# Performance work log

Measured on AMD Instinct MI355X. Metric: run time of the kernel, lower is better.

Reference implementation:

```python
import jax, jax.numpy as jnp
import numpy as np
from functools import partial

B, N, C = 16, 10647, 80   # batch, total anchors (YOLOv3@416), num classes
K = 2048                  # max candidates kept per image before NMS
SCORE_THR = 0.5
IOU_THR = 0.5


def setup_inputs() -> dict:
    key = jax.random.key(0)
    # [B, N, 4+1+C]: xywh (normalized), objectness, class probs
    y_pred = jax.random.uniform(key, (B, N, 5 + C), dtype=jnp.float32)
    return {"y_pred": y_pred}


def _xywh_to_corners(b):
    x, y, w, h = b[..., 0], b[..., 1], b[..., 2], b[..., 3]
    return jnp.stack([x - w / 2, y - h / 2, x + w / 2, y + h / 2], axis=-1)


def _pairwise_iou(boxes):  # boxes [K,4] corners -> [K,K]
    x1, y1, x2, y2 = boxes[:, 0], boxes[:, 1], boxes[:, 2], boxes[:, 3]
    area = jnp.maximum(x2 - x1, 0.0) * jnp.maximum(y2 - y1, 0.0)
    ix1 = jnp.maximum(x1[:, None], x1[None, :])
    iy1 = jnp.maximum(y1[:, None], y1[None, :])
    ix2 = jnp.minimum(x2[:, None], x2[None, :])
    iy2 = jnp.minimum(y2[:, None], y2[None, :])
    inter = jnp.maximum(ix2 - ix1, 0.0) * jnp.maximum(iy2 - iy1, 0.0)
    union = area[:, None] + area[None, :] - inter
    return inter / jnp.maximum(union, 1e-9)


def _greedy_nms_keep(boxes, valid):  # boxes [K,4] sorted by score desc, valid [K] bool
    iou = _pairwise_iou(boxes)
    idxs = jnp.arange(K)

    def body(i, keep):
        suppress = keep[i] & (idxs > i) & (iou[i] > IOU_THR)
        return keep & ~suppress

    return jax.lax.fori_loop(0, K, body, valid)


def reference(y_pred):
    boxes_xywh = y_pred[..., :4]           # [B,N,4]
    obj = y_pred[..., 4]                   # [B,N]
    cls_probs = y_pred[..., 5:]            # [B,N,C]
    scores = obj * jnp.max(cls_probs, axis=-1)  # [B,N]

    # top-K candidates per image (sorted by score desc)
    scores_k, idx = jax.lax.top_k(scores, K)             # [B,K]
    boxes_k = jnp.take_along_axis(boxes_xywh, idx[:, :, None], axis=1)  # [B,K,4]
    corners = _xywh_to_corners(boxes_k)                  # [B,K,4]

    valid = scores_k > SCORE_THR                          # [B,K]
    # NMS keep mask is a non-differentiable selection
    keep = jax.vmap(_greedy_nms_keep)(
        jax.lax.stop_gradient(corners), valid)            # [B,K] bool
    keep_f = keep.astype(scores_k.dtype)

    out_boxes = corners * keep_f[:, :, None]
    out_scores = scores_k * keep_f
    return jnp.concatenate([out_boxes, out_scores[:, :, None]], axis=-1)  # [B,K,5]
```

## Files before the change

kernel.cpp:

```cpp
#include <hip/hip_runtime.h>

#define BATCH 16
#define NROW  10647
#define ROWF  85
#define NCLS  80
#define KTOP  2048
#define MPAD  16384
#define SCORE_THR 0.5f
#define IOU_THR   0.5f

typedef unsigned long long u64;
typedef unsigned int u32;

__device__ __forceinline__ u32 enc_f32(float f) {
    u32 u = __float_as_uint(f);
    return (u & 0x80000000u) ? ~u : (u | 0x80000000u);
}
__device__ __forceinline__ float dec_f32(u32 e) {
    u32 u = (e & 0x80000000u) ? (e & 0x7FFFFFFFu) : ~e;
    return __uint_as_float(u);
}
__device__ __forceinline__ float bcast(float v, int ii) {
    return __uint_as_float(__builtin_amdgcn_readlane(__float_as_uint(v), ii));
}
__device__ __forceinline__ u64 rl64(u64 v, int l) {
    u32 lo = __builtin_amdgcn_readlane((u32)(v & 0xFFFFFFFFull), l);
    u32 hi = __builtin_amdgcn_readlane((u32)(v >> 32), l);
    return ((u64)hi << 32) | (u64)lo;
}
__device__ __forceinline__ void gload_lds16(const void* g, void* lds) {
    __builtin_amdgcn_global_load_lds(
        (const __attribute__((address_space(1))) void*)g,
        (__attribute__((address_space(3))) void*)lds, 16, 0, 0);
}
__device__ __forceinline__ void bar_lds() {
    asm volatile("s_waitcnt lgkmcnt(0)" ::: "memory");
    __builtin_amdgcn_s_barrier();
    __builtin_amdgcn_sched_barrier(0);
}

template<int J>
__device__ __forceinline__ void reg_pass(u64 v[8], int tid, int k) {
    #pragma unroll
    for (int r = 0; r < 8; ++r) {
        if (!(r & J)) {
            bool desc = (((tid * 8 + r) & k) == 0);
            u64 a = v[r], b = v[r | J];
            u64 mx = a > b ? a : b, mn = a > b ? b : a;
            v[r]     = desc ? mx : mn;
            v[r | J] = desc ? mn : mx;
        }
    }
}

__device__ __forceinline__ void shfl_pass(u64 v[8], int tid, int k, int d) {
    const bool upper = (tid & d) == 0;
    const bool desc = (((tid * 8) & k) == 0);
    const bool keepmax = (desc == upper);
    #pragma unroll
    for (int r = 0; r < 8; ++r) {
        u64 pv = __shfl_xor(v[r], d);
        u64 mx = v[r] > pv ? v[r] : pv, mn = v[r] > pv ? pv : v[r];
        v[r] = keepmax ? mx : mn;
    }
}

__device__ __forceinline__ void lds_pass(u64 v[8], int tid, u64* sm, int k, int d) {
    __syncthreads();
    #pragma unroll
    for (int r = 0; r < 8; ++r) sm[r * 256 + tid] = v[r];
    __syncthreads();
    const bool upper = (tid & d) == 0;
    const bool desc = (((tid * 8) & k) == 0);
    const bool keepmax = (desc == upper);
    const int pt = tid ^ d;
    #pragma unroll
    for (int r = 0; r < 8; ++r) {
        u64 pv = sm[r * 256 + pt];
        u64 mx = v[r] > pv ? v[r] : pv, mn = v[r] > pv ? pv : v[r];
        v[r] = keepmax ? mx : mn;
    }
}

__device__ __forceinline__ void sort2048_desc(u64 v[8], int tid, u64* sm) {
    reg_pass<1>(v, tid, 2);
    reg_pass<2>(v, tid, 4); reg_pass<1>(v, tid, 4);
    for (int k = 8; k <= 2048; k <<= 1) {
        for (int j = k >> 1; j >= 8; j >>= 1) {
            int d = j >> 3;
            if (d <= 32) shfl_pass(v, tid, k, d);
            else         lds_pass(v, tid, sm, k, d);
        }
        reg_pass<4>(v, tid, k); reg_pass<2>(v, tid, k); reg_pass<1>(v, tid, k);
    }
}

__device__ __forceinline__ void cleanup2048_desc(u64 v[8], int tid, u64* sm) {
    lds_pass(v, tid, sm, 4096, 128);
    lds_pass(v, tid, sm, 4096, 64);
    for (int d = 32; d >= 1; d >>= 1) shfl_pass(v, tid, 4096, d);
    reg_pass<4>(v, tid, 4096); reg_pass<2>(v, tid, 4096); reg_pass<1>(v, tid, 4096);
}

__global__ void score_kernel(const float* __restrict__ yp, u64* __restrict__ keys) {
    __shared__ float tile[128 * ROWF];
    const int tileIdx = blockIdx.x;
    const int b = blockIdx.y;
    const int tid = threadIdx.x;
    const int batch_lim = NROW * ROWF;
    const int tile_base = tileIdx * 128 * ROWF;

    if (tile_base < batch_lim) {
        const float* src = yp + (long long)b * batch_lim + tile_base;
        int lim_e = batch_lim - tile_base;
        if (lim_e > 128 * ROWF) lim_e = 128 * ROWF;
        const int head = (4 - ((3 * b) & 3)) & 3;
        if (lim_e >= 8) {
            const int nv = (lim_e - head) >> 2;
            for (int e = tid; e < head; e += 256) tile[e] = src[e];
            const float4* s4 = (const float4*)(src + head);
            for (int q = tid; q < nv; q += 256) {
                float4 v = s4[q];
                int o = head + q * 4;
                tile[o] = v.x; tile[o + 1] = v.y; tile[o + 2] = v.z; tile[o + 3] = v.w;
            }
            for (int e = head + nv * 4 + tid; e < lim_e; e += 256) tile[e] = src[e];
        } else {
            for (int e = tid; e < lim_e; e += 256) tile[e] = src[e];
        }
    }
    __syncthreads();

    if (tid < 128) {
        int gr = tileIdx * 128 + tid;
        u64 key = 0ULL;
        if (gr < NROW) {
            const float* r = &tile[tid * ROWF];
            float obj = r[4];
            float m = r[5];
            #pragma unroll
            for (int c = 1; c < NCLS; ++c) m = fmaxf(m, r[5 + c]);
            float s = obj * m;
            key = ((u64)enc_f32(s) << 32) | (u64)(0xFFFFFFFFu - (u32)gr);
        }
        keys[(long long)b * MPAD + gr] = key;
    }
}

__global__ void chunk_sort_kernel(u64* __restrict__ keys) {
    __shared__ u64 sm[2048];
    const int b = blockIdx.y, c = blockIdx.x, tid = threadIdx.x;
    u64* base = keys + (long long)b * MPAD + c * 2048;
    u64 v[8];
    #pragma unroll
    for (int r = 0; r < 8; ++r) v[r] = base[tid * 8 + r];
    sort2048_desc(v, tid, sm);
    #pragma unroll
    for (int r = 0; r < 8; ++r) base[tid * 8 + r] = v[r];
}

__global__ void merge_r1_kernel(const u64* __restrict__ keysA, u64* __restrict__ keysB) {
    __shared__ u64 sm[2048];
    const int b = blockIdx.y, c = blockIdx.x, tid = threadIdx.x;
    const u64* a = keysA + (long long)b * MPAD + c * 4096;
    u64 v[8];
    #pragma unroll
    for (int r = 0; r < 8; ++r) {
        int e = tid * 8 + r;
        u64 va = a[e], vb = a[4095 - e];
        v[r] = va > vb ? va : vb;
    }
    cleanup2048_desc(v, tid, sm);
    u64* d = keysB + (long long)b * MPAD + c * 2048;
    #pragma unroll
    for (int r = 0; r < 8; ++r) d[tid * 8 + r] = v[r];
}

__global__ void merge_r23_gather_kernel(const u64* __restrict__ keysB,
                                        const float* __restrict__ yp,
                                        float* __restrict__ sx1, float* __restrict__ sy1,
                                        float* __restrict__ sx2, float* __restrict__ sy2,
                                        float* __restrict__ sar, float* __restrict__ ssc) {
    __shared__ u64 sm[2048];
    const int b = blockIdx.x, tid = threadIdx.x;
    const u64* a = keysB + (long long)b * MPAD;
    u64 v[8];
    #pragma unroll
    for (int r = 0; r < 8; ++r) {
        int e = tid * 8 + r;
        u64 va = a[e], vb = a[2048 + 2047 - e];
        v[r] = va > vb ? va : vb;
    }
    cleanup2048_desc(v, tid, sm);
    #pragma unroll
    for (int r = 0; r < 8; ++r) {
        int e = tid * 8 + r;
        u64 vb = a[4096 + 2047 - e];
        v[r] = v[r] > vb ? v[r] : vb;
    }
    cleanup2048_desc(v, tid, sm);

    #pragma unroll
    for (int r = 0; r < 8; ++r) {
        u64 key = v[r];
        float s = dec_f32((u32)(key >> 32));
        u32 idx = 0xFFFFFFFFu - (u32)(key & 0xFFFFFFFFu);
        const float* rp = yp + (long long)b * NROW * ROWF + (long long)idx * ROWF;
        float x = rp[0], y = rp[1], w = rp[2], h = rp[3];
        float hx = w * 0.5f, hy = h * 0.5f;
        float a1 = x - hx, b1 = y - hy, a2 = x + hx, b2 = y + hy;
        int o = b * KTOP + tid * 8 + r;
        sx1[o] = a1; sy1[o] = b1; sx2[o] = a2; sy2[o] = b2;
        sar[o] = fmaxf(a2 - a1, 0.f) * fmaxf(b2 - b1, 0.f);
        ssc[o] = s;
    }
}

__global__ void mask_kernel(const float* __restrict__ sx1, const float* __restrict__ sy1,
                            const float* __restrict__ sx2, const float* __restrict__ sy2,
                            const float* __restrict__ sar, u64* __restrict__ mask,
                            u64* __restrict__ diag) {
    const int b = blockIdx.y;
    const int t = blockIdx.x * 4 + (threadIdx.x >> 6);
    const int lane = threadIdx.x & 63;

    int rb = (int)((65.0f - sqrtf(4225.0f - 8.0f * (float)t)) * 0.5f);
    while (rb * (65 - rb) / 2 > t) --rb;
    while ((rb + 1) * (64 - rb) / 2 <= t) ++rb;
    const int cb = rb + t - rb * (65 - rb) / 2;

    const int oi = b * KTOP + rb * 64 + lane;
    const int oj = b * KTOP + cb * 64 + lane;
    const float rx1 = sx1[oi], ry1 = sy1[oi], rx2 = sx2[oi], ry2 = sy2[oi], ra = sar[oi];
    const float cx1 = sx1[oj], cy1 = sy1[oj], cx2 = sx2[oj], cy2 = sy2[oj], ca = sar[oj];
    const bool dg = (rb == cb);

    u64 myword = 0ULL;
    for (int ii = 0; ii < 64; ++ii) {
        float ax1 = bcast(rx1, ii), ay1 = bcast(ry1, ii);
        float ax2 = bcast(rx2, ii), ay2 = bcast(ry2, ii);
        float aa  = bcast(ra,  ii);
        float ix1 = fmaxf(ax1, cx1);
        float iy1 = fmaxf(ay1, cy1);
        float ix2 = fminf(ax2, cx2);
        float iy2 = fminf(ay2, cy2);
        float inter = fmaxf(ix2 - ix1, 0.f) * fmaxf(iy2 - iy1, 0.f);
        float uni = aa + ca - inter;
        float iou = inter / fmaxf(uni, 1e-9f);
        bool cond = (iou > IOU_THR) && (!dg || (lane > ii));
        u64 bal = __ballot(cond);
        if (lane == ii) myword = bal;
    }
    mask[(long long)(b * KTOP + rb * 64 + lane) * 32 + cb] = myword;
    if (dg) diag[(long long)b * 2048 + rb * 64 + lane] = myword;
}

__global__ void nms_out_kernel(const float* __restrict__ sx1, const float* __restrict__ sy1,
                               const float* __restrict__ sx2, const float* __restrict__ sy2,
                               const float* __restrict__ ssc,
                               const u64* __restrict__ mask,
                               const u64* __restrict__ diag, float* __restrict__ out) {
    __shared__ u64 slots[4][2048];
    __shared__ u64 pend[8][32];
    __shared__ u64 curs;
    __shared__ u64 sbits64[32];
    __shared__ u64 keepw[32];
    const int b = blockIdx.x;
    const int tid = threadIdx.x;
    const int lane = tid & 63;
    const int wave = tid >> 6;
    const u64* mb = mask + (long long)(b * KTOP) * 32;
    const char* mbc = (const char*)mb;
    const u64* dg = diag + (long long)b * 2048;

    auto issue_block = [&](int B) {
        const char* src = mbc + (size_t)B * 16384;
        char* dst = (char*)&slots[B & 3][0];
        #pragma unroll
        for (int i = 0; i < 16; ++i)
            gload_lds16(src + i * 1024 + lane * 16, dst + i * 1024);
    };

    {
        const float* sp = ssc + b * KTOP + tid * 8;
        float4 sa = *(const float4*)(sp);
        float4 sb = *(const float4*)(sp + 4);
        unsigned bits =
            (unsigned)(sa.x > SCORE_THR)       | ((unsigned)(sa.y > SCORE_THR) << 1) |
            ((unsigned)(sa.z > SCORE_THR) << 2) | ((unsigned)(sa.w > SCORE_THR) << 3) |
            ((unsigned)(sb.x > SCORE_THR) << 4) | ((unsigned)(sb.y > SCORE_THR) << 5) |
            ((unsigned)(sb.z > SCORE_THR) << 6) | ((unsigned)(sb.w > SCORE_THR) << 7);
        ((unsigned char*)sbits64)[tid] = (unsigned char)bits;
    }
    u64 dia = 0ULL;
    if (wave == 0) dia = dg[lane];
    if (wave >= 1) issue_block(wave - 1);
    __syncthreads();

    u64 myw = 0ULL;
    if (wave == 0 && lane < 32) myw = sbits64[lane];

    #pragma unroll 1
    for (int w = 0; w < 32; ++w) {
        const u64* blk = &slots[w & 3][0];

        if (wave == 0) {
            u64 dia_next = 0ULL;
            if (w < 31) dia_next = dg[(w + 1) * 64 + lane];
            u64 cur = rl64(myw, w);
            #pragma unroll
            for (int p = 0; p < 4; ++p) {
                u64 dd[16];
                #pragma unroll
                for (int i = 0; i < 16; ++i) dd[i] = rl64(dia, p * 16 + i);
                #pragma unroll
                for (int i = 0; i < 16; ++i) {
                    u64 m = ((cur >> (p * 16 + i)) & 1ULL) ? dd[i] : 0ULL;
                    cur &= ~m;
                }
            }
            if (lane == 0) curs = cur;
            dia = dia_next;
        } else {
            const int rr = wave - 1;
            if ((w % 3) == rr && w + 3 < 32) issue_block(w + 3);
            if (((w + 1) % 3) == rr)
                asm volatile("s_waitcnt vmcnt(0)" ::: "memory");
        }
        bar_lds();

        {
            u64 curv = curs;
            const int col = tid & 31;
            const int rg  = tid >> 5;
            const u64* rp = blk + (size_t)rg * 256 + col;
            u32 bits8 = (u32)(curv >> (rg * 8)) & 0xFFu;
            u64 acc = 0ULL;
            #pragma unroll
            for (int i = 0; i < 8; ++i) {
                u64 t = rp[(size_t)i * 32];
                acc |= ((bits8 >> i) & 1u) ? t : 0ULL;
            }
            pend[rg][col] = acc;
        }
        bar_lds();

        if (wave == 0 && lane < 32) {
            u64 cur = curs;
            u64 s = ((pend[0][lane] | pend[1][lane]) | (pend[2][lane] | pend[3][lane]))
                  | ((pend[4][lane] | pend[5][lane]) | (pend[6][lane] | pend[7][lane]));
            if (lane == w) myw = cur;
            else if (lane > w) myw &= ~s;
        }
    }

    if (wave == 0 && lane < 32) keepw[lane] = myw;
    __syncthreads();

    for (int t = tid; t < KTOP; t += 256) {
        int o = b * KTOP + t;
        float f = ((keepw[t >> 6] >> (t & 63)) & 1ULL) ? 1.0f : 0.0f;
        float* op = out + (long long)o * 5;
        op[0] = sx1[o] * f;
        op[1] = sy1[o] * f;
        op[2] = sx2[o] * f;
        op[3] = sy2[o] * f;
        op[4] = ssc[o] * f;
    }
}

extern "C" void kernel_launch(void* const* d_in, const int* in_sizes, int n_in,
                              void* d_out, int out_size, void* d_ws, size_t ws_size,
                              hipStream_t stream) {
    const float* yp = (const float*)d_in[0];
    float* out = (float*)d_out;
    char* ws = (char*)d_ws;

    const size_t KEYS_BYTES = (size_t)BATCH * MPAD * sizeof(u64);
    const size_t MASK_BYTES = (size_t)BATCH * KTOP * 32 * sizeof(u64);
    const size_t SOA_BYTES  = (size_t)6 * BATCH * KTOP * sizeof(float);
    u64* keysA = (u64*)ws;
    u64* keysB = (u64*)(ws + KEYS_BYTES);
    u64* mask  = (u64*)ws;
    float* soa = (float*)(ws + MASK_BYTES);
    u64* diag  = (u64*)(ws + MASK_BYTES + SOA_BYTES);
    const int SA = BATCH * KTOP;
    float* sx1 = soa + 0 * SA;
    float* sy1 = soa + 1 * SA;
    float* sx2 = soa + 2 * SA;
    float* sy2 = soa + 3 * SA;
    float* sar = soa + 4 * SA;
    float* ssc = soa + 5 * SA;

    score_kernel<<<dim3(96, BATCH), 256, 0, stream>>>(yp, keysA);
    chunk_sort_kernel<<<dim3(6, BATCH), 256, 0, stream>>>(keysA);
    merge_r1_kernel<<<dim3(3, BATCH), 256, 0, stream>>>(keysA, keysB);
    merge_r23_gather_kernel<<<BATCH, 256, 0, stream>>>(keysB, yp,
                                                       sx1, sy1, sx2, sy2, sar, ssc);
    mask_kernel<<<dim3(132, BATCH), 256, 0, stream>>>(sx1, sy1, sx2, sy2, sar, mask, diag);
    nms_out_kernel<<<BATCH, 256, 0, stream>>>(sx1, sy1, sx2, sy2, ssc, mask, diag, out);
}
```

Baseline: 161.3 us.

## Process two 64-box NMS blocks per iteration using super-diagonal mask

The mask kernel now also stores the super-diagonal tile (row block i against column block i+1). The serial NMS loop uses it to resolve two consecutive 64-candidate blocks per iteration, which halves the iterations and the number of block-wide barriers. The mask prefetch is reorganised to load two blocks at a time into the four LDS slots. In exchange, wave 0 does more serial readlane work per iteration and the kernel needs extra workspace for the super-diagonal words.

```diff
diff --git a/kernel.cpp b/kernel.cpp
--- a/kernel.cpp
+++ b/kernel.cpp
@@ -219,7 +219,7 @@
 __global__ void mask_kernel(const float* __restrict__ sx1, const float* __restrict__ sy1,
                             const float* __restrict__ sx2, const float* __restrict__ sy2,
                             const float* __restrict__ sar, u64* __restrict__ mask,
-                            u64* __restrict__ diag) {
+                            u64* __restrict__ diag, u64* __restrict__ nxt) {
     const int b = blockIdx.y;
     const int t = blockIdx.x * 4 + (threadIdx.x >> 6);
     const int lane = threadIdx.x & 63;
@@ -253,16 +253,18 @@
     }
     mask[(long long)(b * KTOP + rb * 64 + lane) * 32 + cb] = myword;
     if (dg) diag[(long long)b * 2048 + rb * 64 + lane] = myword;
+    if (cb == rb + 1) nxt[(long long)b * 2048 + rb * 64 + lane] = myword;
 }
 
 __global__ void nms_out_kernel(const float* __restrict__ sx1, const float* __restrict__ sy1,
                                const float* __restrict__ sx2, const float* __restrict__ sy2,
                                const float* __restrict__ ssc,
                                const u64* __restrict__ mask,
-                               const u64* __restrict__ diag, float* __restrict__ out) {
+                               const u64* __restrict__ diag,
+                               const u64* __restrict__ nxt, float* __restrict__ out) {
     __shared__ u64 slots[4][2048];
     __shared__ u64 pend[8][32];
-    __shared__ u64 curs;
+    __shared__ u64 cursAB[2];
     __shared__ u64 sbits64[32];
     __shared__ u64 keepw[32];
     const int b = blockIdx.x;
@@ -272,14 +274,7 @@
     const u64* mb = mask + (long long)(b * KTOP) * 32;
     const char* mbc = (const char*)mb;
     const u64* dg = diag + (long long)b * 2048;
-
-    auto issue_block = [&](int B) {
-        const char* src = mbc + (size_t)B * 16384;
-        char* dst = (char*)&slots[B & 3][0];
-        #pragma unroll
-        for (int i = 0; i < 16; ++i)
-            gload_lds16(src + i * 1024 + lane * 16, dst + i * 1024);
-    };
+    const u64* nx = nxt + (long long)b * 2048;
 
     {
         const float* sp = ssc + b * KTOP + tid * 8;
@@ -292,66 +287,119 @@
             ((unsigned)(sb.z > SCORE_THR) << 6) | ((unsigned)(sb.w > SCORE_THR) << 7);
         ((unsigned char*)sbits64)[tid] = (unsigned char)bits;
     }
-    u64 dia = 0ULL;
-    if (wave == 0) dia = dg[lane];
-    if (wave >= 1) issue_block(wave - 1);
+    u64 diaA = 0ULL, diaB = 0ULL, nxtA = 0ULL;
+    if (wave == 0) {
+        diaA = dg[lane];
+        diaB = dg[64 + lane];
+        nxtA = nx[lane];
+    } else {
+        const int rr = wave - 1;
+        for (int i = rr; i < 32; i += 3) {
+            int B = i >> 4, c = i & 15;
+            gload_lds16(mbc + (size_t)B * 16384 + c * 1024 + lane * 16,
+                        (char*)&slots[B][0] + c * 1024);
+        }
+    }
     __syncthreads();
 
     u64 myw = 0ULL;
     if (wave == 0 && lane < 32) myw = sbits64[lane];
 
     #pragma unroll 1
-    for (int w = 0; w < 32; ++w) {
-        const u64* blk = &slots[w & 3][0];
+    for (int k = 0; k < 16; ++k) {
+        const int A = 2 * k, B = 2 * k + 1;
 
         if (wave == 0) {
-            u64 dia_next = 0ULL;
-            if (w < 31) dia_next = dg[(w + 1) * 64 + lane];
-            u64 cur = rl64(myw, w);
+            u64 diaA_n = 0ULL, diaB_n = 0ULL, nxtA_n = 0ULL;
+            if (k < 15) {
+                diaA_n = dg[(A + 2) * 64 + lane];
+                diaB_n = dg[(A + 3) * 64 + lane];
+                nxtA_n = nx[(A + 2) * 64 + lane];
+            }
+            if (k > 0 && lane < 32 && lane >= A) {
+                u64 s = ((pend[0][lane] | pend[1][lane]) | (pend[2][lane] | pend[3][lane]))
+                      | ((pend[4][lane] | pend[5][lane]) | (pend[6][lane] | pend[7][lane]));
+                myw &= ~s;
+            }
+            u64 curA = rl64(myw, A);
             #pragma unroll
             for (int p = 0; p < 4; ++p) {
                 u64 dd[16];
                 #pragma unroll
-                for (int i = 0; i < 16; ++i) dd[i] = rl64(dia, p * 16 + i);
+                for (int i = 0; i < 16; ++i) dd[i] = rl64(diaA, p * 16 + i);
                 #pragma unroll
                 for (int i = 0; i < 16; ++i) {
-                    u64 m = ((cur >> (p * 16 + i)) & 1ULL) ? dd[i] : 0ULL;
-                    cur &= ~m;
+                    u64 m = ((curA >> (p * 16 + i)) & 1ULL) ? dd[i] : 0ULL;
+                    curA &= ~m;
                 }
             }
-            if (lane == 0) curs = cur;
-            dia = dia_next;
+            u64 s0 = 0, s1 = 0, s2 = 0, s3 = 0;
+            #pragma unroll
+            for (int p = 0; p < 4; ++p) {
+                u64 nn[16];
+                #pragma unroll
+                for (int i = 0; i < 16; ++i) nn[i] = rl64(nxtA, p * 16 + i);
+                #pragma unroll
+                for (int i = 0; i < 16; ++i) {
+                    u64 m = ((curA >> (p * 16 + i)) & 1ULL) ? nn[i] : 0ULL;
+                    if ((i & 3) == 0) s0 |= m;
+                    else if ((i & 3) == 1) s1 |= m;
+                    else if ((i & 3) == 2) s2 |= m;
+                    else s3 |= m;
+                }
+            }
+            u64 curB = rl64(myw, B) & ~((s0 | s1) | (s2 | s3));
+            #pragma unroll
+            for (int p = 0; p < 4; ++p) {
+                u64 dd[16];
+                #pragma unroll
+                for (int i = 0; i < 16; ++i) dd[i] = rl64(diaB, p * 16 + i);
+                #pragma unroll
+                for (int i = 0; i < 16; ++i) {
+                    u64 m = ((curB >> (p * 16 + i)) & 1ULL) ? dd[i] : 0ULL;
+                    curB &= ~m;
+                }
+            }
+            if (lane == 0) { cursAB[0] = curA; cursAB[1] = curB; }
+            if (lane == A) myw = curA;
+            if (lane == B) myw = curB;
+            diaA = diaA_n; diaB = diaB_n; nxtA = nxtA_n;
         } else {
-            const int rr = wave - 1;
-            if ((w % 3) == rr && w + 3 < 32) issue_block(w + 3);
-            if (((w + 1) % 3) == rr)
+            if (k > 0)
                 asm volatile("s_waitcnt vmcnt(0)" ::: "memory");
+            if (k < 15) {
+                const int rr = wave - 1;
+                for (int i = rr; i < 32; i += 3) {
+                    int Bb = A + 2 + (i >> 4), c = i & 15;
+                    gload_lds16(mbc + (size_t)Bb * 16384 + c * 1024 + lane * 16,
+                                (char*)&slots[Bb & 3][0] + c * 1024);
+                }
+            }
         }
         bar_lds();
 
         {
-            u64 curv = curs;
+            u64 cA = cursAB[0], cB = cursAB[1];
             const int col = tid & 31;
             const int rg  = tid >> 5;
-            const u64* rp = blk + (size_t)rg * 256 + col;
-            u32 bits8 = (u32)(curv >> (rg * 8)) & 0xFFu;
+            const u64* rpA = &slots[A & 3][0] + (size_t)rg * 256 + col;
+            const u64* rpB = &slots[B & 3][0] + (size_t)rg * 256 + col;
+            u32 bA = (u32)(cA >> (rg * 8)) & 0xFFu;
+            u32 bB = (u32)(cB >> (rg * 8)) & 0xFFu;
             u64 acc = 0ULL;
             #pragma unroll
             for (int i = 0; i < 8; ++i) {
-                u64 t = rp[(size_t)i * 32];
-                acc |= ((bits8 >> i) & 1u) ? t : 0ULL;
+                u64 tA = rpA[(size_t)i * 32];
+                acc |= ((bA >> i) & 1u) ? tA : 0ULL;
+            }
+            #pragma unroll
+            for (int i = 0; i < 8; ++i) {
+                u64 tB = rpB[(size_t)i * 32];
+                acc |= ((bB >> i) & 1u) ? tB : 0ULL;
             }
             pend[rg][col] = acc;
         }
         bar_lds();
-
-        if (wave == 0 && lane < 32) {
-            u64 cur = curs;
-            u64 s = ((pend[0][lane] | pend[1][lane]) | (pend[2][lane] | pend[3][lane]))
-                  | ((pend[4][lane] | pend[5][lane]) | (pend[6][lane] | pend[7][lane]));
-            if (lane == w) myw = cur;
-            else if (lane > w) myw &= ~s;
-        }
     }
 
     if (wave == 0 && lane < 32) keepw[lane] = myw;
@@ -379,11 +427,13 @@
     const size_t KEYS_BYTES = (size_t)BATCH * MPAD * sizeof(u64);
     const size_t MASK_BYTES = (size_t)BATCH * KTOP * 32 * sizeof(u64);
     const size_t SOA_BYTES  = (size_t)6 * BATCH * KTOP * sizeof(float);
+    const size_t DIAG_BYTES = (size_t)BATCH * 2048 * sizeof(u64);
     u64* keysA = (u64*)ws;
     u64* keysB = (u64*)(ws + KEYS_BYTES);
     u64* mask  = (u64*)ws;
     float* soa = (float*)(ws + MASK_BYTES);
     u64* diag  = (u64*)(ws + MASK_BYTES + SOA_BYTES);
+    u64* nxt   = (u64*)(ws + MASK_BYTES + SOA_BYTES + DIAG_BYTES);
     const int SA = BATCH * KTOP;
     float* sx1 = soa + 0 * SA;
     float* sy1 = soa + 1 * SA;
@@ -397,6 +447,8 @@
     merge_r1_kernel<<<dim3(3, BATCH), 256, 0, stream>>>(keysA, keysB);
     merge_r23_gather_kernel<<<BATCH, 256, 0, stream>>>(keysB, yp,
                                                        sx1, sy1, sx2, sy2, sar, ssc);
-    mask_kernel<<<dim3(132, BATCH), 256, 0, stream>>>(sx1, sy1, sx2, sy2, sar, mask, diag);
-    nms_out_kernel<<<BATCH, 256, 0, stream>>>(sx1, sy1, sx2, sy2, ssc, mask, diag, out);
-}
+    mask_kernel<<<dim3(132, BATCH), 256, 0, stream>>>(sx1, sy1, sx2, sy2, sar,
+                                                      mask, diag, nxt);
+    nms_out_kernel<<<BATCH, 256, 0, stream>>>(sx1, sy1, sx2, sy2, ssc,
+                                              mask, diag, nxt, out);
+}
```

Result: slower. 178.5 us (+10.6%).
